# Kernel tuning notes

Measured on AMD Instinct MI355X. Metric: run time of the kernel, lower is better.

Reference implementation:

```python
import jax, jax.numpy as jnp
import numpy as np

B, T = 512, 200
N_SKILLS, M, DK, DV, H = 1000, 50, 64, 64, 128


def setup_inputs() -> dict:
    key = jax.random.key(0)
    ks = jax.random.split(key, 12)
    inp = {
        'skill_seq': jax.random.randint(ks[0], (B, T), 0, N_SKILLS, dtype=jnp.int32),
        'correct_seq': jax.random.randint(ks[1], (B, T), 0, 2, dtype=jnp.int32),
        'mask': jnp.ones((B, T), dtype=jnp.float32),
        'skill_embed': jax.random.normal(ks[2], (N_SKILLS, DK), dtype=jnp.float32),
        'key_memory': jax.random.normal(ks[3], (M, DK), dtype=jnp.float32) * 0.1,
        'value_init': jnp.zeros((M, DV), dtype=jnp.float32),
        'interaction_embed': jax.random.normal(ks[4], (2 * N_SKILLS, DV), dtype=jnp.float32),
        'erase_W': jax.random.normal(ks[5], (DV, DV), dtype=jnp.float32) * 0.05,
        'erase_b': jnp.zeros((DV,), dtype=jnp.float32),
        'add_W': jax.random.normal(ks[6], (DV, DV), dtype=jnp.float32) * 0.05,
        'add_b': jnp.zeros((DV,), dtype=jnp.float32),
        'fc1_W': jax.random.normal(ks[7], (DK + DV, H), dtype=jnp.float32) * 0.05,
        'fc1_b': jnp.zeros((H,), dtype=jnp.float32),
        'fc2_W': jax.random.normal(ks[8], (H, 1), dtype=jnp.float32) * 0.05,
        'fc2_b': jnp.zeros((1,), dtype=jnp.float32),
    }
    return inp


def reference(skill_seq, correct_seq, mask, skill_embed, key_memory, value_init,
              interaction_embed, erase_W, erase_b, add_W, add_b,
              fc1_W, fc1_b, fc2_W, fc2_b):
    n_skills = skill_embed.shape[0]
    b = skill_seq.shape[0]
    # Time-invariant-per-step quantities are precomputed vectorized over (B,T):
    q = skill_embed[skill_seq]                                   # (B,T,dk)
    w = jax.nn.softmax(jnp.einsum('btk,mk->btm', q, key_memory), axis=-1)  # (B,T,M)
    v = interaction_embed[skill_seq + correct_seq * n_skills]    # (B,T,dv)
    e = jax.nn.sigmoid(v @ erase_W + erase_b)                    # (B,T,dv)
    a = jnp.tanh(v @ add_W + add_b)                              # (B,T,dv)

    def step(mem, inputs):
        # mem: (B,M,dv); read BEFORE write, matching the torch loop
        w_t, e_t, a_t = inputs                                   # (B,M),(B,dv),(B,dv)
        read = jnp.einsum('bm,bmv->bv', w_t, mem)                # (B,dv)
        we = w_t[:, :, None]                                     # (B,M,1)
        mem = mem * (1.0 - we * e_t[:, None, :]) + we * a_t[:, None, :]
        return mem, read

    mem0 = jnp.broadcast_to(value_init, (b,) + value_init.shape)
    _, reads = jax.lax.scan(step, mem0,
                            (jnp.swapaxes(w, 0, 1), jnp.swapaxes(e, 0, 1), jnp.swapaxes(a, 0, 1)))
    reads = jnp.swapaxes(reads, 0, 1)                            # (B,T,dv)

    x = jnp.concatenate([q, reads], axis=-1)                     # (B,T,dk+dv)
    h = jax.nn.relu(x @ fc1_W + fc1_b)
    logit = (h @ fc2_W + fc2_b)[..., 0]
    p = jax.nn.sigmoid(logit)
    return p * mask, correct_seq.astype(jnp.float32) * mask
```

## Files before the change

### kernel.cpp

```cpp
#include <hip/hip_runtime.h>
#include <hip/hip_bf16.h>

#define B_  512
#define T_  200
#define NS  1000
#define M_  50
#define DK  64
#define DV  64
#define H_  128
#define NPOS (B_ * T_)

typedef __hip_bfloat16 bf16;
typedef unsigned short ushort_t;
typedef __bf16 bf16x8 __attribute__((ext_vector_type(8)));
typedef float  f32x4  __attribute__((ext_vector_type(4)));

__device__ __forceinline__ float ldf(const void* p, int i, int isbf) {
    return isbf ? __bfloat162float(((const bf16*)p)[i]) : ((const float*)p)[i];
}
__device__ __forceinline__ int sniff(const void* mask) {
    return (*(const unsigned*)mask == 0x3F800000u) ? 0 : 1;
}
__device__ __forceinline__ float rl(float x, int l) {
    return __int_as_float(__builtin_amdgcn_readlane(__float_as_int(x), l));
}
__device__ __forceinline__ ushort_t f2bf(float v) {
    bf16 h = __float2bfloat16(v);
    return *(ushort_t*)&h;
}

__global__ __launch_bounds__(256) void dk19_tabs(
    const void* __restrict__ mask,
    const void* __restrict__ skill_embed, const void* __restrict__ key_memory,
    const void* __restrict__ inter,
    const void* __restrict__ eW, const void* __restrict__ eb,
    const void* __restrict__ aW, const void* __restrict__ ab,
    const void* __restrict__ fc1W, const void* __restrict__ fc1b,
    float* __restrict__ w_tab, unsigned* __restrict__ ea_tab,
    float* __restrict__ hq_tab, ushort_t* __restrict__ W2f) {
    int isbf = sniff(mask);
    int lane = threadIdx.x & 63;
    int gwid = (blockIdx.x << 2) | (threadIdx.x >> 6);

    if (gwid < NS) {
        int s = gwid;
        float q = ldf(skill_embed, s * DK + lane, isbf);
        float acc = 0.f;
        if (lane < M_) {
            #pragma unroll 16
            for (int k = 0; k < DK; ++k)
                acc = fmaf(rl(q, k), ldf(key_memory, lane * DK + k, isbf), acc);
        }
        float val = (lane < M_) ? acc : -1e30f;
        float mx = val;
        #pragma unroll
        for (int off = 1; off < 64; off <<= 1) mx = fmaxf(mx, __shfl_xor(mx, off, 64));
        float ex = (lane < M_) ? __expf(val - mx) : 0.f;
        float sm = ex;
        #pragma unroll
        for (int off = 1; off < 64; off <<= 1) sm += __shfl_xor(sm, off, 64);
        w_tab[s * 64 + lane] = (lane < M_) ? ex / sm : 0.f;
    } else if (gwid < 3 * NS) {
        int r = gwid - NS;
        float vv = ldf(inter, r * DV + lane, isbf);
        float eacc = ldf(eb, lane, isbf);
        float aacc = ldf(ab, lane, isbf);
        #pragma unroll 16
        for (int u = 0; u < DV; ++u) {
            float vu = rl(vv, u);
            eacc = fmaf(vu, ldf(eW, u * DV + lane, isbf), eacc);
            aacc = fmaf(vu, ldf(aW, u * DV + lane, isbf), aacc);
        }
        float ev = 1.f / (1.f + __expf(-eacc));
        float av = tanhf(aacc);
        ea_tab[r * 64 + lane] = ((unsigned)f2bf(av) << 16) | (unsigned)f2bf(ev);
    } else if (gwid < 4 * NS) {
        int s = gwid - 3 * NS;
        float q = ldf(skill_embed, s * DK + lane, isbf);
        float acc0 = ldf(fc1b, lane, isbf);
        float acc1 = ldf(fc1b, 64 + lane, isbf);
        #pragma unroll 16
        for (int k = 0; k < DK; ++k) {
            float qk = rl(q, k);
            acc0 = fmaf(qk, ldf(fc1W, k * H_ + lane, isbf), acc0);
            acc1 = fmaf(qk, ldf(fc1W, k * H_ + 64 + lane, isbf), acc1);
        }
        hq_tab[s * H_ + lane]      = acc0;
        hq_tab[s * H_ + 64 + lane] = acc1;
    } else if (gwid < 4 * NS + 64) {
        int f = gwid - 4 * NS;
        int tile = f >> 3, kk = f & 7;
        int n = tile * 16 + (lane & 15);
        #pragma unroll
        for (int j = 0; j < 8; ++j) {
            int v = (kk * 32 + (lane >> 4) * 8 + j) & 63;
            W2f[(f * 64 + lane) * 8 + j] = f2bf(ldf(fc1W, (DK + v) * H_ + n, isbf));
        }
    }
}

template<int KS>
__global__ __launch_bounds__(64, 2) void dk19_scan(
    const int*  __restrict__ ss, const int* __restrict__ cs,
    const void* __restrict__ mask, const void* __restrict__ value_init,
    const float* __restrict__ w_tab, const unsigned* __restrict__ ea_tab,
    ushort_t* __restrict__ read_bf) {

    constexpr int NW = 16 / KS;
    int isbf = sniff(mask);
    int lane = threadIdx.x;
    int bk   = blockIdx.x;
    int b    = bk / KS, k = bk - b * KS;
    const int base = b * T_;
    const int row0 = (64 / KS) * k;
    const float4* w4 = (const float4*)w_tab;

    float4 mem[NW];
    #pragma unroll
    for (int i = 0; i < NW; ++i) {
        int r = row0 + 4 * i;
        mem[i].x = (r + 0 < M_) ? ldf(value_init, (r + 0) * DV + lane, isbf) : 0.f;
        mem[i].y = (r + 1 < M_) ? ldf(value_init, (r + 1) * DV + lane, isbf) : 0.f;
        mem[i].z = (r + 2 < M_) ? ldf(value_init, (r + 2) * DV + lane, isbf) : 0.f;
        mem[i].w = (r + 3 < M_) ? ldf(value_init, (r + 3) * DV + lane, isbf) : 0.f;
    }

    int s2 = ss[base + 2], c2 = cs[base + 2];
    int s3 = ss[base + 3], c3 = cs[base + 3];

    float4 wa[NW], wb[NW];
    unsigned eaA, eaB;
    {
        int sA = ss[base], cA = cs[base];
        eaA = ea_tab[(sA + cA * NS) * 64 + lane];
        #pragma unroll
        for (int i = 0; i < NW; ++i) wa[i] = w4[sA * 16 + NW * k + i];
        int sB = ss[base + 1], cB = cs[base + 1];
        eaB = ea_tab[(sB + cB * NS) * 64 + lane];
        #pragma unroll
        for (int i = 0; i < NW; ++i) wb[i] = w4[sB * 16 + NW * k + i];
    }

    for (int t = 0; t < T_; t += 2) {
        {
            float e0 = __uint_as_float(eaA << 16);
            float a0 = __uint_as_float(eaA & 0xFFFF0000u);
            float acc0 = 0.f, acc1 = 0.f, acc2 = 0.f, acc3 = 0.f;
            #pragma unroll
            for (int i = 0; i < NW; ++i) {
                float4 w = wa[i];
                acc0 = fmaf(w.x, mem[i].x, acc0);
                acc1 = fmaf(w.y, mem[i].y, acc1);
                acc2 = fmaf(w.z, mem[i].z, acc2);
                acc3 = fmaf(w.w, mem[i].w, acc3);
                mem[i].x = fmaf(-w.x, fmaf(e0, mem[i].x, -a0), mem[i].x);
                mem[i].y = fmaf(-w.y, fmaf(e0, mem[i].y, -a0), mem[i].y);
                mem[i].z = fmaf(-w.z, fmaf(e0, mem[i].z, -a0), mem[i].z);
                mem[i].w = fmaf(-w.w, fmaf(e0, mem[i].w, -a0), mem[i].w);
            }
            read_bf[((size_t)(base + t) * KS + k) * 64 + lane] =
                f2bf((acc0 + acc1) + (acc2 + acc3));
        }
        {
            eaA = ea_tab[(s2 + c2 * NS) * 64 + lane];
            #pragma unroll
            for (int i = 0; i < NW; ++i) wa[i] = w4[s2 * 16 + NW * k + i];
        }
        s2 = s3; c2 = c3;
        int tf = (t + 4 < T_) ? t + 4 : T_ - 1;
        s3 = ss[base + tf]; c3 = cs[base + tf];

        {
            float e1 = __uint_as_float(eaB << 16);
            float a1 = __uint_as_float(eaB & 0xFFFF0000u);
            float acc0 = 0.f, acc1 = 0.f, acc2 = 0.f, acc3 = 0.f;
            #pragma unroll
            for (int i = 0; i < NW; ++i) {
                float4 w = wb[i];
                acc0 = fmaf(w.x, mem[i].x, acc0);
                acc1 = fmaf(w.y, mem[i].y, acc1);
                acc2 = fmaf(w.z, mem[i].z, acc2);
                acc3 = fmaf(w.w, mem[i].w, acc3);
                mem[i].x = fmaf(-w.x, fmaf(e1, mem[i].x, -a1), mem[i].x);
                mem[i].y = fmaf(-w.y, fmaf(e1, mem[i].y, -a1), mem[i].y);
                mem[i].z = fmaf(-w.z, fmaf(e1, mem[i].z, -a1), mem[i].z);
                mem[i].w = fmaf(-w.w, fmaf(e1, mem[i].w, -a1), mem[i].w);
            }
            read_bf[((size_t)(base + t + 1) * KS + k) * 64 + lane] =
                f2bf((acc0 + acc1) + (acc2 + acc3));
        }
        {
            eaB = ea_tab[(s2 + c2 * NS) * 64 + lane];
            #pragma unroll
            for (int i = 0; i < NW; ++i) wb[i] = w4[s2 * 16 + NW * k + i];
        }
        s2 = s3; c2 = c3;
        tf = (t + 5 < T_) ? t + 5 : T_ - 1;
        s3 = ss[base + tf]; c3 = cs[base + tf];
    }
}

#define FOR8(X) X(0) X(1) X(2) X(3) X(4) X(5) X(6) X(7)
#define DECL_BT(t) bf16x8 b##t##_0, b##t##_1, b##t##_2, b##t##_3, \
                          b##t##_4, b##t##_5, b##t##_6, b##t##_7;
#define LOAD_BT(t) \
    b##t##_0 = B8[((t)*8+0)*64+lane]; b##t##_1 = B8[((t)*8+1)*64+lane]; \
    b##t##_2 = B8[((t)*8+2)*64+lane]; b##t##_3 = B8[((t)*8+3)*64+lane]; \
    b##t##_4 = B8[((t)*8+4)*64+lane]; b##t##_5 = B8[((t)*8+5)*64+lane]; \
    b##t##_6 = B8[((t)*8+6)*64+lane]; b##t##_7 = B8[((t)*8+7)*64+lane];
#define DECL_C(t)  f32x4 c##t = {0.f, 0.f, 0.f, 0.f};
#define LOAD_A(kk) bf16x8 a##kk = A8[col * 32 + (kk) * 4 + quad];
#define MFMA_KK(kk) \
    c0 = __builtin_amdgcn_mfma_f32_16x16x32_bf16(a##kk, b0_##kk, c0, 0, 0, 0); \
    c1 = __builtin_amdgcn_mfma_f32_16x16x32_bf16(a##kk, b1_##kk, c1, 0, 0, 0); \
    c2 = __builtin_amdgcn_mfma_f32_16x16x32_bf16(a##kk, b2_##kk, c2, 0, 0, 0); \
    c3 = __builtin_amdgcn_mfma_f32_16x16x32_bf16(a##kk, b3_##kk, c3, 0, 0, 0); \
    c4 = __builtin_amdgcn_mfma_f32_16x16x32_bf16(a##kk, b4_##kk, c4, 0, 0, 0); \
    c5 = __builtin_amdgcn_mfma_f32_16x16x32_bf16(a##kk, b5_##kk, c5, 0, 0, 0); \
    c6 = __builtin_amdgcn_mfma_f32_16x16x32_bf16(a##kk, b6_##kk, c6, 0, 0, 0); \
    c7 = __builtin_amdgcn_mfma_f32_16x16x32_bf16(a##kk, b7_##kk, c7, 0, 0, 0);
#define EPI(t) { \
    float h; \
    h = c##t.x + hq_tab[s0r * H_ + t * 16 + col]; x0 = fmaf(fmaxf(h, 0.f), f2w##t, x0); \
    h = c##t.y + hq_tab[s1r * H_ + t * 16 + col]; x1 = fmaf(fmaxf(h, 0.f), f2w##t, x1); \
    h = c##t.z + hq_tab[s2r * H_ + t * 16 + col]; x2 = fmaf(fmaxf(h, 0.f), f2w##t, x2); \
    h = c##t.w + hq_tab[s3r * H_ + t * 16 + col]; x3 = fmaf(fmaxf(h, 0.f), f2w##t, x3); }

__global__ __launch_bounds__(64)
__attribute__((amdgpu_waves_per_eu(1))) void dk19_fc4(
    const int*  __restrict__ skill_seq, const int* __restrict__ correct_seq,
    const void* __restrict__ mask,
    const void* __restrict__ fc2W, const void* __restrict__ fc2b,
    const float* __restrict__ hq_tab, const ushort_t* __restrict__ W2f,
    const ushort_t* __restrict__ read_bf,
    float* __restrict__ out0, float* __restrict__ out1) {

    int isbf = sniff(mask);
    int lane = threadIdx.x;
    int col  = lane & 15, quad = lane >> 4;

    const bf16x8* B8 = (const bf16x8*)W2f;
    DECL_BT(0) DECL_BT(1) DECL_BT(2) DECL_BT(3)
    DECL_BT(4) DECL_BT(5) DECL_BT(6) DECL_BT(7)
    FOR8(LOAD_BT)

    float f2w0 = ldf(fc2W,   0 + col, isbf), f2w1 = ldf(fc2W,  16 + col, isbf);
    float f2w2 = ldf(fc2W,  32 + col, isbf), f2w3 = ldf(fc2W,  48 + col, isbf);
    float f2w4 = ldf(fc2W,  64 + col, isbf), f2w5 = ldf(fc2W,  80 + col, isbf);
    float f2w6 = ldf(fc2W,  96 + col, isbf), f2w7 = ldf(fc2W, 112 + col, isbf);
    float f2b  = ldf(fc2b, 0, isbf);

    for (int pg = blockIdx.x; pg < NPOS / 16; pg += gridDim.x) {
        int p0 = pg * 16;
        const bf16x8* A8 = (const bf16x8*)(read_bf + (size_t)p0 * 256);
        LOAD_A(0) LOAD_A(1) LOAD_A(2) LOAD_A(3)
        LOAD_A(4) LOAD_A(5) LOAD_A(6) LOAD_A(7)

        int s0r = skill_seq[p0 + quad * 4 + 0];
        int s1r = skill_seq[p0 + quad * 4 + 1];
        int s2r = skill_seq[p0 + quad * 4 + 2];
        int s3r = skill_seq[p0 + quad * 4 + 3];

        FOR8(DECL_C)
        FOR8(MFMA_KK)

        float x0 = 0.f, x1 = 0.f, x2 = 0.f, x3 = 0.f;
        FOR8(EPI)

        #pragma unroll
        for (int off = 1; off < 16; off <<= 1) {
            x0 += __shfl_xor(x0, off, 64);
            x1 += __shfl_xor(x1, off, 64);
            x2 += __shfl_xor(x2, off, 64);
            x3 += __shfl_xor(x3, off, 64);
        }

        float mk0 = ldf(mask, p0 + quad * 4 + 0, isbf);
        float mk1 = ldf(mask, p0 + quad * 4 + 1, isbf);
        float mk2 = ldf(mask, p0 + quad * 4 + 2, isbf);
        float mk3 = ldf(mask, p0 + quad * 4 + 3, isbf);
        if (col == 0) {
            out0[p0 + quad * 4 + 0] = mk0 / (1.f + __expf(-(x0 + f2b)));
            out0[p0 + quad * 4 + 1] = mk1 / (1.f + __expf(-(x1 + f2b)));
            out0[p0 + quad * 4 + 2] = mk2 / (1.f + __expf(-(x2 + f2b)));
            out0[p0 + quad * 4 + 3] = mk3 / (1.f + __expf(-(x3 + f2b)));
        }
        if (col == 1) {
            out1[p0 + quad * 4 + 0] = (float)correct_seq[p0 + quad * 4 + 0] * mk0;
            out1[p0 + quad * 4 + 1] = (float)correct_seq[p0 + quad * 4 + 1] * mk1;
            out1[p0 + quad * 4 + 2] = (float)correct_seq[p0 + quad * 4 + 2] * mk2;
            out1[p0 + quad * 4 + 3] = (float)correct_seq[p0 + quad * 4 + 3] * mk3;
        }
    }
}

#define FCKK_G(kk) { \
    bf16x8 av = A8[col * (8 * KS) + (kk) * 4 + quad]; \
    c0 = __builtin_amdgcn_mfma_f32_16x16x32_bf16(av, B8[(0 * 8 + (kk)) * 64 + lane], c0, 0, 0, 0); \
    c1 = __builtin_amdgcn_mfma_f32_16x16x32_bf16(av, B8[(1 * 8 + (kk)) * 64 + lane], c1, 0, 0, 0); \
    c2 = __builtin_amdgcn_mfma_f32_16x16x32_bf16(av, B8[(2 * 8 + (kk)) * 64 + lane], c2, 0, 0, 0); \
    c3 = __builtin_amdgcn_mfma_f32_16x16x32_bf16(av, B8[(3 * 8 + (kk)) * 64 + lane], c3, 0, 0, 0); \
    c4 = __builtin_amdgcn_mfma_f32_16x16x32_bf16(av, B8[(4 * 8 + (kk)) * 64 + lane], c4, 0, 0, 0); \
    c5 = __builtin_amdgcn_mfma_f32_16x16x32_bf16(av, B8[(5 * 8 + (kk)) * 64 + lane], c5, 0, 0, 0); \
    c6 = __builtin_amdgcn_mfma_f32_16x16x32_bf16(av, B8[(6 * 8 + (kk)) * 64 + lane], c6, 0, 0, 0); \
    c7 = __builtin_amdgcn_mfma_f32_16x16x32_bf16(av, B8[(7 * 8 + (kk)) * 64 + lane], c7, 0, 0, 0); }

template<int KS>
__global__ __launch_bounds__(256) void dk19_fcgen(
    const int*  __restrict__ skill_seq, const int* __restrict__ correct_seq,
    const void* __restrict__ mask,
    const void* __restrict__ fc2W, const void* __restrict__ fc2b,
    const float* __restrict__ hq_tab, const ushort_t* __restrict__ W2f,
    const ushort_t* __restrict__ read_bf,
    float* __restrict__ out0, float* __restrict__ out1) {

    int isbf = sniff(mask);
    int lane = threadIdx.x & 63;
    int wid  = (blockIdx.x << 2) | (threadIdx.x >> 6);
    int p0   = wid * 16;
    int col  = lane & 15, quad = lane >> 4;

    const bf16x8* B8 = (const bf16x8*)W2f;
    const bf16x8* A8 = (const bf16x8*)(read_bf + (size_t)p0 * (64 * KS));

    FOR8(DECL_C)
    FCKK_G(0) FCKK_G(1) FCKK_G(2) FCKK_G(3)

    float f2w0 = ldf(fc2W,   0 + col, isbf), f2w1 = ldf(fc2W,  16 + col, isbf);
    float f2w2 = ldf(fc2W,  32 + col, isbf), f2w3 = ldf(fc2W,  48 + col, isbf);
    float f2w4 = ldf(fc2W,  64 + col, isbf), f2w5 = ldf(fc2W,  80 + col, isbf);
    float f2w6 = ldf(fc2W,  96 + col, isbf), f2w7 = ldf(fc2W, 112 + col, isbf);
    float f2b  = ldf(fc2b, 0, isbf);

    int s0r = skill_seq[p0 + quad * 4 + 0];
    int s1r = skill_seq[p0 + quad * 4 + 1];
    int s2r = skill_seq[p0 + quad * 4 + 2];
    int s3r = skill_seq[p0 + quad * 4 + 3];

    float x0 = 0.f, x1 = 0.f, x2 = 0.f, x3 = 0.f;
    FOR8(EPI)

    #pragma unroll
    for (int off = 1; off < 16; off <<= 1) {
        x0 += __shfl_xor(x0, off, 64);
        x1 += __shfl_xor(x1, off, 64);
        x2 += __shfl_xor(x2, off, 64);
        x3 += __shfl_xor(x3, off, 64);
    }

    float mk0 = ldf(mask, p0 + quad * 4 + 0, isbf);
    float mk1 = ldf(mask, p0 + quad * 4 + 1, isbf);
    float mk2 = ldf(mask, p0 + quad * 4 + 2, isbf);
    float mk3 = ldf(mask, p0 + quad * 4 + 3, isbf);
    if (col == 0) {
        out0[p0 + quad * 4 + 0] = mk0 / (1.f + __expf(-(x0 + f2b)));
        out0[p0 + quad * 4 + 1] = mk1 / (1.f + __expf(-(x1 + f2b)));
        out0[p0 + quad * 4 + 2] = mk2 / (1.f + __expf(-(x2 + f2b)));
        out0[p0 + quad * 4 + 3] = mk3 / (1.f + __expf(-(x3 + f2b)));
    }
    if (col == 1) {
        out1[p0 + quad * 4 + 0] = (float)correct_seq[p0 + quad * 4 + 0] * mk0;
        out1[p0 + quad * 4 + 1] = (float)correct_seq[p0 + quad * 4 + 1] * mk1;
        out1[p0 + quad * 4 + 2] = (float)correct_seq[p0 + quad * 4 + 2] * mk2;
        out1[p0 + quad * 4 + 3] = (float)correct_seq[p0 + quad * 4 + 3] * mk3;
    }
}

extern "C" void kernel_launch(void* const* d_in, const int* in_sizes, int n_in,
                              void* d_out, int out_size, void* d_ws, size_t ws_size,
                              hipStream_t stream) {
    const int*  skill_seq   = (const int*)d_in[0];
    const int*  correct_seq = (const int*)d_in[1];
    const void* mask        = d_in[2];
    const void* skill_embed = d_in[3];
    const void* key_memory  = d_in[4];
    const void* value_init  = d_in[5];
    const void* inter       = d_in[6];
    const void* erase_W     = d_in[7];
    const void* erase_b     = d_in[8];
    const void* add_W       = d_in[9];
    const void* add_b       = d_in[10];
    const void* fc1_W       = d_in[11];
    const void* fc1_b       = d_in[12];
    const void* fc2_W       = d_in[13];
    const void* fc2_b       = d_in[14];
    float* out = (float*)d_out;

    float*    ws      = (float*)d_ws + 16;
    float*    w_tab   = ws;
    unsigned* ea_tab  = (unsigned*)(ws + 64000);
    float*    hq_tab  = ws + 192000;
    ushort_t* W2f     = (ushort_t*)(ws + 320000);
    ushort_t* read_bf = (ushort_t*)(ws + 336400);

    dk19_tabs<<<1016, 256, 0, stream>>>(mask, skill_embed, key_memory, inter,
                                        erase_W, erase_b, add_W, add_b,
                                        fc1_W, fc1_b,
                                        w_tab, ea_tab, hq_tab, W2f);

    if (ws_size >= (size_t)54 * 1000 * 1000) {
        dk19_scan<4><<<B_ * 4, 64, 0, stream>>>(skill_seq, correct_seq, mask, value_init,
                                                w_tab, ea_tab, read_bf);
        dk19_fc4<<<1024, 64, 0, stream>>>(skill_seq, correct_seq, mask,
                                          fc2_W, fc2_b, hq_tab, W2f, read_bf,
                                          out, out + (size_t)NPOS);
    } else {
        dk19_scan<2><<<B_ * 2, 64, 0, stream>>>(skill_seq, correct_seq, mask, value_init,
                                                w_tab, ea_tab, read_bf);
        dk19_fcgen<2><<<1600, 256, 0, stream>>>(skill_seq, correct_seq, mask,
                                                fc2_W, fc2_b, hq_tab, W2f, read_bf,
                                                out, out + (size_t)NPOS);
    }
}
```

Measured before the change: 181.1 us.

## Split scan memory rows across 8 waves per batch with LDS reduction

The scan kernel now uses one 512-thread block per batch row, with 8 waves each owning 8 memory rows. Partial reads are reduced through shared memory in 8-step chunks with double buffering, so only the full fp32 read vector is written as bf16. Before, 4 separate blocks each wrote a bf16 partial that the FC kernel summed through extra K. This shrinks read_bf traffic, lets the FC kernel drop to K=64 (2 MFMAs per tile) with more waves, and removes the workspace-size fallback path. The cost is a block-wide barrier every 8 steps of a latency-bound recurrence.

```diff
diff --git a/kernel.cpp b/kernel.cpp
--- a/kernel.cpp
+++ b/kernel.cpp
@@ -29,7 +29,7 @@
     return *(ushort_t*)&h;
 }
 
-__global__ __launch_bounds__(256) void dk19_tabs(
+__global__ __launch_bounds__(256) void dk20_tabs(
     const void* __restrict__ mask,
     const void* __restrict__ skill_embed, const void* __restrict__ key_memory,
     const void* __restrict__ inter,
@@ -87,37 +87,70 @@
         }
         hq_tab[s * H_ + lane]      = acc0;
         hq_tab[s * H_ + 64 + lane] = acc1;
-    } else if (gwid < 4 * NS + 64) {
+    } else if (gwid < 4 * NS + 16) {
         int f = gwid - 4 * NS;
-        int tile = f >> 3, kk = f & 7;
+        int tile = f >> 1, kk = f & 1;
         int n = tile * 16 + (lane & 15);
         #pragma unroll
         for (int j = 0; j < 8; ++j) {
-            int v = (kk * 32 + (lane >> 4) * 8 + j) & 63;
+            int v = kk * 32 + (lane >> 4) * 8 + j;
             W2f[(f * 64 + lane) * 8 + j] = f2bf(ldf(fc1W, (DK + v) * H_ + n, isbf));
         }
     }
 }
 
-template<int KS>
-__global__ __launch_bounds__(64, 2) void dk19_scan(
+#define SCAN_STEP(EA, WARR, TP) { \
+    float e0 = __uint_as_float((EA) << 16); \
+    float a0 = __uint_as_float((EA) & 0xFFFF0000u); \
+    float acc0 = 0.f, acc1 = 0.f, acc2 = 0.f, acc3 = 0.f; \
+    _Pragma("unroll") \
+    for (int i = 0; i < 2; ++i) { \
+        float4 w = WARR[i]; \
+        acc0 = fmaf(w.x, mem[i].x, acc0); \
+        acc1 = fmaf(w.y, mem[i].y, acc1); \
+        acc2 = fmaf(w.z, mem[i].z, acc2); \
+        acc3 = fmaf(w.w, mem[i].w, acc3); \
+        mem[i].x = fmaf(-w.x, fmaf(e0, mem[i].x, -a0), mem[i].x); \
+        mem[i].y = fmaf(-w.y, fmaf(e0, mem[i].y, -a0), mem[i].y); \
+        mem[i].z = fmaf(-w.z, fmaf(e0, mem[i].z, -a0), mem[i].z); \
+        mem[i].w = fmaf(-w.w, fmaf(e0, mem[i].w, -a0), mem[i].w); \
+    } \
+    red[buf][k][TP][lane] = (acc0 + acc1) + (acc2 + acc3); }
+
+#define REFILL(EA, WARR) { \
+    EA = ea_tab[(s2 + c2 * NS) * 64 + lane]; \
+    WARR[0] = w4[s2 * 16 + 2 * k]; \
+    WARR[1] = w4[s2 * 16 + 2 * k + 1]; }
+
+#define ADV(TF) { s2 = s3; c2 = c3; int tf_ = (TF) < T_ ? (TF) : T_ - 1; \
+    s3 = ss[base + tf_]; c3 = cs[base + tf_]; }
+
+#define SUMSTORE(PB, CC) { \
+    float s_ = red[PB][0][k][lane] + red[PB][1][k][lane] \
+             + red[PB][2][k][lane] + red[PB][3][k][lane] \
+             + red[PB][4][k][lane] + red[PB][5][k][lane] \
+             + red[PB][6][k][lane] + red[PB][7][k][lane]; \
+    read_bf[(size_t)(base + (CC) * 8 + k) * 64 + lane] = f2bf(s_); }
+
+__global__ __launch_bounds__(512, 4) void dk20_scan(
     const int*  __restrict__ ss, const int* __restrict__ cs,
     const void* __restrict__ mask, const void* __restrict__ value_init,
     const float* __restrict__ w_tab, const unsigned* __restrict__ ea_tab,
     ushort_t* __restrict__ read_bf) {
 
-    constexpr int NW = 16 / KS;
+    __shared__ float red[2][8][8][64];
+
     int isbf = sniff(mask);
-    int lane = threadIdx.x;
-    int bk   = blockIdx.x;
-    int b    = bk / KS, k = bk - b * KS;
+    int lane = threadIdx.x & 63;
+    int k    = threadIdx.x >> 6;
+    int b    = blockIdx.x;
     const int base = b * T_;
-    const int row0 = (64 / KS) * k;
+    const int row0 = 8 * k;
     const float4* w4 = (const float4*)w_tab;
 
-    float4 mem[NW];
+    float4 mem[2];
     #pragma unroll
-    for (int i = 0; i < NW; ++i) {
+    for (int i = 0; i < 2; ++i) {
         int r = row0 + 4 * i;
         mem[i].x = (r + 0 < M_) ? ldf(value_init, (r + 0) * DV + lane, isbf) : 0.f;
         mem[i].y = (r + 1 < M_) ? ldf(value_init, (r + 1) * DV + lane, isbf) : 0.f;
@@ -128,97 +161,42 @@
     int s2 = ss[base + 2], c2 = cs[base + 2];
     int s3 = ss[base + 3], c3 = cs[base + 3];
 
-    float4 wa[NW], wb[NW];
+    float4 wa[2], wb[2];
     unsigned eaA, eaB;
     {
         int sA = ss[base], cA = cs[base];
         eaA = ea_tab[(sA + cA * NS) * 64 + lane];
-        #pragma unroll
-        for (int i = 0; i < NW; ++i) wa[i] = w4[sA * 16 + NW * k + i];
+        wa[0] = w4[sA * 16 + 2 * k]; wa[1] = w4[sA * 16 + 2 * k + 1];
         int sB = ss[base + 1], cB = cs[base + 1];
         eaB = ea_tab[(sB + cB * NS) * 64 + lane];
-        #pragma unroll
-        for (int i = 0; i < NW; ++i) wb[i] = w4[sB * 16 + NW * k + i];
-    }
-
-    for (int t = 0; t < T_; t += 2) {
-        {
-            float e0 = __uint_as_float(eaA << 16);
-            float a0 = __uint_as_float(eaA & 0xFFFF0000u);
-            float acc0 = 0.f, acc1 = 0.f, acc2 = 0.f, acc3 = 0.f;
-            #pragma unroll
-            for (int i = 0; i < NW; ++i) {
-                float4 w = wa[i];
-                acc0 = fmaf(w.x, mem[i].x, acc0);
-                acc1 = fmaf(w.y, mem[i].y, acc1);
-                acc2 = fmaf(w.z, mem[i].z, acc2);
-                acc3 = fmaf(w.w, mem[i].w, acc3);
-                mem[i].x = fmaf(-w.x, fmaf(e0, mem[i].x, -a0), mem[i].x);
-                mem[i].y = fmaf(-w.y, fmaf(e0, mem[i].y, -a0), mem[i].y);
-                mem[i].z = fmaf(-w.z, fmaf(e0, mem[i].z, -a0), mem[i].z);
-                mem[i].w = fmaf(-w.w, fmaf(e0, mem[i].w, -a0), mem[i].w);
-            }
-            read_bf[((size_t)(base + t) * KS + k) * 64 + lane] =
-                f2bf((acc0 + acc1) + (acc2 + acc3));
-        }
-        {
-            eaA = ea_tab[(s2 + c2 * NS) * 64 + lane];
-            #pragma unroll
-            for (int i = 0; i < NW; ++i) wa[i] = w4[s2 * 16 + NW * k + i];
-        }
-        s2 = s3; c2 = c3;
-        int tf = (t + 4 < T_) ? t + 4 : T_ - 1;
-        s3 = ss[base + tf]; c3 = cs[base + tf];
-
-        {
-            float e1 = __uint_as_float(eaB << 16);
-            float a1 = __uint_as_float(eaB & 0xFFFF0000u);
-            float acc0 = 0.f, acc1 = 0.f, acc2 = 0.f, acc3 = 0.f;
-            #pragma unroll
-            for (int i = 0; i < NW; ++i) {
-                float4 w = wb[i];
-                acc0 = fmaf(w.x, mem[i].x, acc0);
-                acc1 = fmaf(w.y, mem[i].y, acc1);
-                acc2 = fmaf(w.z, mem[i].z, acc2);
-                acc3 = fmaf(w.w, mem[i].w, acc3);
-                mem[i].x = fmaf(-w.x, fmaf(e1, mem[i].x, -a1), mem[i].x);
-                mem[i].y = fmaf(-w.y, fmaf(e1, mem[i].y, -a1), mem[i].y);
-                mem[i].z = fmaf(-w.z, fmaf(e1, mem[i].z, -a1), mem[i].z);
-                mem[i].w = fmaf(-w.w, fmaf(e1, mem[i].w, -a1), mem[i].w);
-            }
-            read_bf[((size_t)(base + t + 1) * KS + k) * 64 + lane] =
-                f2bf((acc0 + acc1) + (acc2 + acc3));
-        }
-        {
-            eaB = ea_tab[(s2 + c2 * NS) * 64 + lane];
-            #pragma unroll
-            for (int i = 0; i < NW; ++i) wb[i] = w4[s2 * 16 + NW * k + i];
-        }
-        s2 = s3; c2 = c3;
-        tf = (t + 5 < T_) ? t + 5 : T_ - 1;
-        s3 = ss[base + tf]; c3 = cs[base + tf];
-    }
+        wb[0] = w4[sB * 16 + 2 * k]; wb[1] = w4[sB * 16 + 2 * k + 1];
+    }
+
+    for (int c = 0; c < 25; ++c) {
+        int buf = c & 1;
+        #pragma unroll
+        for (int tp = 0; tp < 8; tp += 2) {
+            int t = c * 8 + tp;
+            SCAN_STEP(eaA, wa, tp)
+            REFILL(eaA, wa)
+            ADV(t + 4)
+            SCAN_STEP(eaB, wb, tp + 1)
+            REFILL(eaB, wb)
+            ADV(t + 5)
+        }
+        if (c > 0) SUMSTORE((c - 1) & 1, c - 1)
+        __syncthreads();
+    }
+    SUMSTORE(0, 24)
 }
 
 #define FOR8(X) X(0) X(1) X(2) X(3) X(4) X(5) X(6) X(7)
-#define DECL_BT(t) bf16x8 b##t##_0, b##t##_1, b##t##_2, b##t##_3, \
-                          b##t##_4, b##t##_5, b##t##_6, b##t##_7;
-#define LOAD_BT(t) \
-    b##t##_0 = B8[((t)*8+0)*64+lane]; b##t##_1 = B8[((t)*8+1)*64+lane]; \
-    b##t##_2 = B8[((t)*8+2)*64+lane]; b##t##_3 = B8[((t)*8+3)*64+lane]; \
-    b##t##_4 = B8[((t)*8+4)*64+lane]; b##t##_5 = B8[((t)*8+5)*64+lane]; \
-    b##t##_6 = B8[((t)*8+6)*64+lane]; b##t##_7 = B8[((t)*8+7)*64+lane];
 #define DECL_C(t)  f32x4 c##t = {0.f, 0.f, 0.f, 0.f};
-#define LOAD_A(kk) bf16x8 a##kk = A8[col * 32 + (kk) * 4 + quad];
-#define MFMA_KK(kk) \
-    c0 = __builtin_amdgcn_mfma_f32_16x16x32_bf16(a##kk, b0_##kk, c0, 0, 0, 0); \
-    c1 = __builtin_amdgcn_mfma_f32_16x16x32_bf16(a##kk, b1_##kk, c1, 0, 0, 0); \
-    c2 = __builtin_amdgcn_mfma_f32_16x16x32_bf16(a##kk, b2_##kk, c2, 0, 0, 0); \
-    c3 = __builtin_amdgcn_mfma_f32_16x16x32_bf16(a##kk, b3_##kk, c3, 0, 0, 0); \
-    c4 = __builtin_amdgcn_mfma_f32_16x16x32_bf16(a##kk, b4_##kk, c4, 0, 0, 0); \
-    c5 = __builtin_amdgcn_mfma_f32_16x16x32_bf16(a##kk, b5_##kk, c5, 0, 0, 0); \
-    c6 = __builtin_amdgcn_mfma_f32_16x16x32_bf16(a##kk, b6_##kk, c6, 0, 0, 0); \
-    c7 = __builtin_amdgcn_mfma_f32_16x16x32_bf16(a##kk, b7_##kk, c7, 0, 0, 0);
+#define LOADB(t) bf16x8 b##t##_0 = B8[(2 * (t)) * 64 + lane], \
+                        b##t##_1 = B8[(2 * (t) + 1) * 64 + lane];
+#define MFMA2(t) \
+    c##t = __builtin_amdgcn_mfma_f32_16x16x32_bf16(a0, b##t##_0, c##t, 0, 0, 0); \
+    c##t = __builtin_amdgcn_mfma_f32_16x16x32_bf16(a1, b##t##_1, c##t, 0, 0, 0);
 #define EPI(t) { \
     float h; \
     h = c##t.x + hq_tab[s0r * H_ + t * 16 + col]; x0 = fmaf(fmaxf(h, 0.f), f2w##t, x0); \
@@ -227,7 +205,7 @@
     h = c##t.w + hq_tab[s3r * H_ + t * 16 + col]; x3 = fmaf(fmaxf(h, 0.f), f2w##t, x3); }
 
 __global__ __launch_bounds__(64)
-__attribute__((amdgpu_waves_per_eu(1))) void dk19_fc4(
+__attribute__((amdgpu_waves_per_eu(3))) void dk20_fc(
     const int*  __restrict__ skill_seq, const int* __restrict__ correct_seq,
     const void* __restrict__ mask,
     const void* __restrict__ fc2W, const void* __restrict__ fc2b,
@@ -240,9 +218,7 @@
     int col  = lane & 15, quad = lane >> 4;
 
     const bf16x8* B8 = (const bf16x8*)W2f;
-    DECL_BT(0) DECL_BT(1) DECL_BT(2) DECL_BT(3)
-    DECL_BT(4) DECL_BT(5) DECL_BT(6) DECL_BT(7)
-    FOR8(LOAD_BT)
+    FOR8(LOADB)
 
     float f2w0 = ldf(fc2W,   0 + col, isbf), f2w1 = ldf(fc2W,  16 + col, isbf);
     float f2w2 = ldf(fc2W,  32 + col, isbf), f2w3 = ldf(fc2W,  48 + col, isbf);
@@ -252,9 +228,9 @@
 
     for (int pg = blockIdx.x; pg < NPOS / 16; pg += gridDim.x) {
         int p0 = pg * 16;
-        const bf16x8* A8 = (const bf16x8*)(read_bf + (size_t)p0 * 256);
-        LOAD_A(0) LOAD_A(1) LOAD_A(2) LOAD_A(3)
-        LOAD_A(4) LOAD_A(5) LOAD_A(6) LOAD_A(7)
+        const bf16x8* A8 = (const bf16x8*)(read_bf + (size_t)p0 * 64);
+        bf16x8 a0 = A8[col * 8 + quad];
+        bf16x8 a1 = A8[col * 8 + 4 + quad];
 
         int s0r = skill_seq[p0 + quad * 4 + 0];
         int s1r = skill_seq[p0 + quad * 4 + 1];
@@ -262,7 +238,7 @@
         int s3r = skill_seq[p0 + quad * 4 + 3];
 
         FOR8(DECL_C)
-        FOR8(MFMA_KK)
+        FOR8(MFMA2)
 
         float x0 = 0.f, x1 = 0.f, x2 = 0.f, x3 = 0.f;
         FOR8(EPI)
@@ -291,78 +267,6 @@
             out1[p0 + quad * 4 + 2] = (float)correct_seq[p0 + quad * 4 + 2] * mk2;
             out1[p0 + quad * 4 + 3] = (float)correct_seq[p0 + quad * 4 + 3] * mk3;
         }
-    }
-}
-
-#define FCKK_G(kk) { \
-    bf16x8 av = A8[col * (8 * KS) + (kk) * 4 + quad]; \
-    c0 = __builtin_amdgcn_mfma_f32_16x16x32_bf16(av, B8[(0 * 8 + (kk)) * 64 + lane], c0, 0, 0, 0); \
-    c1 = __builtin_amdgcn_mfma_f32_16x16x32_bf16(av, B8[(1 * 8 + (kk)) * 64 + lane], c1, 0, 0, 0); \
-    c2 = __builtin_amdgcn_mfma_f32_16x16x32_bf16(av, B8[(2 * 8 + (kk)) * 64 + lane], c2, 0, 0, 0); \
-    c3 = __builtin_amdgcn_mfma_f32_16x16x32_bf16(av, B8[(3 * 8 + (kk)) * 64 + lane], c3, 0, 0, 0); \
-    c4 = __builtin_amdgcn_mfma_f32_16x16x32_bf16(av, B8[(4 * 8 + (kk)) * 64 + lane], c4, 0, 0, 0); \
-    c5 = __builtin_amdgcn_mfma_f32_16x16x32_bf16(av, B8[(5 * 8 + (kk)) * 64 + lane], c5, 0, 0, 0); \
-    c6 = __builtin_amdgcn_mfma_f32_16x16x32_bf16(av, B8[(6 * 8 + (kk)) * 64 + lane], c6, 0, 0, 0); \
-    c7 = __builtin_amdgcn_mfma_f32_16x16x32_bf16(av, B8[(7 * 8 + (kk)) * 64 + lane], c7, 0, 0, 0); }
-
-template<int KS>
-__global__ __launch_bounds__(256) void dk19_fcgen(
-    const int*  __restrict__ skill_seq, const int* __restrict__ correct_seq,
-    const void* __restrict__ mask,
-    const void* __restrict__ fc2W, const void* __restrict__ fc2b,
-    const float* __restrict__ hq_tab, const ushort_t* __restrict__ W2f,
-    const ushort_t* __restrict__ read_bf,
-    float* __restrict__ out0, float* __restrict__ out1) {
-
-    int isbf = sniff(mask);
-    int lane = threadIdx.x & 63;
-    int wid  = (blockIdx.x << 2) | (threadIdx.x >> 6);
-    int p0   = wid * 16;
-    int col  = lane & 15, quad = lane >> 4;
-
-    const bf16x8* B8 = (const bf16x8*)W2f;
-    const bf16x8* A8 = (const bf16x8*)(read_bf + (size_t)p0 * (64 * KS));
-
-    FOR8(DECL_C)
-    FCKK_G(0) FCKK_G(1) FCKK_G(2) FCKK_G(3)
-
-    float f2w0 = ldf(fc2W,   0 + col, isbf), f2w1 = ldf(fc2W,  16 + col, isbf);
-    float f2w2 = ldf(fc2W,  32 + col, isbf), f2w3 = ldf(fc2W,  48 + col, isbf);
-    float f2w4 = ldf(fc2W,  64 + col, isbf), f2w5 = ldf(fc2W,  80 + col, isbf);
-    float f2w6 = ldf(fc2W,  96 + col, isbf), f2w7 = ldf(fc2W, 112 + col, isbf);
-    float f2b  = ldf(fc2b, 0, isbf);
-
-    int s0r = skill_seq[p0 + quad * 4 + 0];
-    int s1r = skill_seq[p0 + quad * 4 + 1];
-    int s2r = skill_seq[p0 + quad * 4 + 2];
-    int s3r = skill_seq[p0 + quad * 4 + 3];
-
-    float x0 = 0.f, x1 = 0.f, x2 = 0.f, x3 = 0.f;
-    FOR8(EPI)
-
-    #pragma unroll
-    for (int off = 1; off < 16; off <<= 1) {
-        x0 += __shfl_xor(x0, off, 64);
-        x1 += __shfl_xor(x1, off, 64);
-        x2 += __shfl_xor(x2, off, 64);
-        x3 += __shfl_xor(x3, off, 64);
-    }
-
-    float mk0 = ldf(mask, p0 + quad * 4 + 0, isbf);
-    float mk1 = ldf(mask, p0 + quad * 4 + 1, isbf);
-    float mk2 = ldf(mask, p0 + quad * 4 + 2, isbf);
-    float mk3 = ldf(mask, p0 + quad * 4 + 3, isbf);
-    if (col == 0) {
-        out0[p0 + quad * 4 + 0] = mk0 / (1.f + __expf(-(x0 + f2b)));
-        out0[p0 + quad * 4 + 1] = mk1 / (1.f + __expf(-(x1 + f2b)));
-        out0[p0 + quad * 4 + 2] = mk2 / (1.f + __expf(-(x2 + f2b)));
-        out0[p0 + quad * 4 + 3] = mk3 / (1.f + __expf(-(x3 + f2b)));
-    }
-    if (col == 1) {
-        out1[p0 + quad * 4 + 0] = (float)correct_seq[p0 + quad * 4 + 0] * mk0;
-        out1[p0 + quad * 4 + 1] = (float)correct_seq[p0 + quad * 4 + 1] * mk1;
-        out1[p0 + quad * 4 + 2] = (float)correct_seq[p0 + quad * 4 + 2] * mk2;
-        out1[p0 + quad * 4 + 3] = (float)correct_seq[p0 + quad * 4 + 3] * mk3;
     }
 }
 
@@ -393,22 +297,15 @@
     ushort_t* W2f     = (ushort_t*)(ws + 320000);
     ushort_t* read_bf = (ushort_t*)(ws + 336400);
 
-    dk19_tabs<<<1016, 256, 0, stream>>>(mask, skill_embed, key_memory, inter,
+    dk20_tabs<<<1004, 256, 0, stream>>>(mask, skill_embed, key_memory, inter,
                                         erase_W, erase_b, add_W, add_b,
                                         fc1_W, fc1_b,
                                         w_tab, ea_tab, hq_tab, W2f);
 
-    if (ws_size >= (size_t)54 * 1000 * 1000) {
-        dk19_scan<4><<<B_ * 4, 64, 0, stream>>>(skill_seq, correct_seq, mask, value_init,
-                                                w_tab, ea_tab, read_bf);
-        dk19_fc4<<<1024, 64, 0, stream>>>(skill_seq, correct_seq, mask,
-                                          fc2_W, fc2_b, hq_tab, W2f, read_bf,
-                                          out, out + (size_t)NPOS);
-    } else {
-        dk19_scan<2><<<B_ * 2, 64, 0, stream>>>(skill_seq, correct_seq, mask, value_init,
-                                                w_tab, ea_tab, read_bf);
-        dk19_fcgen<2><<<1600, 256, 0, stream>>>(skill_seq, correct_seq, mask,
-                                                fc2_W, fc2_b, hq_tab, W2f, read_bf,
-                                                out, out + (size_t)NPOS);
-    }
-}
+    dk20_scan<<<B_, 512, 0, stream>>>(skill_seq, correct_seq, mask, value_init,
+                                      w_tab, ea_tab, read_bf);
+
+    dk20_fc<<<3200, 64, 0, stream>>>(skill_seq, correct_seq, mask,
+                                     fc2_W, fc2_b, hq_tab, W2f, read_bf,
+                                     out, out + (size_t)NPOS);
+}
```

Measured after the change: 180.6 us. About the same (-0.3%).

## Shrink fc kernel B-register footprint, vectorize hq gathers, raise occupancy

Applied to the files above, without the earlier changes.

The fc kernel no longer holds all 64 B fragments in registers. The W2f layout now has 16 fragments, with the K offset folded via modulo in the old packing, so only 16 bf16x8 registers are kept. The hq table is stored transposed per column, so each lane fetches its 8 hq values with two float4 loads instead of 32 scalar gathers. The kernel uses waves_per_eu(3) with a 3200-block grid, and the ws_size fallback path is removed. This trades register-resident weights for higher occupancy and fewer load instructions, which risks correctness if the KS=4 read layout does not match the repacked B indexing.

```diff
diff --git a/kernel.cpp b/kernel.cpp
--- a/kernel.cpp
+++ b/kernel.cpp
@@ -29,7 +29,7 @@
     return *(ushort_t*)&h;
 }
 
-__global__ __launch_bounds__(256) void dk19_tabs(
+__global__ __launch_bounds__(256) void dk26_tabs(
     const void* __restrict__ mask,
     const void* __restrict__ skill_embed, const void* __restrict__ key_memory,
     const void* __restrict__ inter,
@@ -37,7 +37,7 @@
     const void* __restrict__ aW, const void* __restrict__ ab,
     const void* __restrict__ fc1W, const void* __restrict__ fc1b,
     float* __restrict__ w_tab, unsigned* __restrict__ ea_tab,
-    float* __restrict__ hq_tab, ushort_t* __restrict__ W2f) {
+    float* __restrict__ hq2, ushort_t* __restrict__ W2f) {
     int isbf = sniff(mask);
     int lane = threadIdx.x & 63;
     int gwid = (blockIdx.x << 2) | (threadIdx.x >> 6);
@@ -85,22 +85,22 @@
             acc0 = fmaf(qk, ldf(fc1W, k * H_ + lane, isbf), acc0);
             acc1 = fmaf(qk, ldf(fc1W, k * H_ + 64 + lane, isbf), acc1);
         }
-        hq_tab[s * H_ + lane]      = acc0;
-        hq_tab[s * H_ + 64 + lane] = acc1;
-    } else if (gwid < 4 * NS + 64) {
+        hq2[s * H_ + (lane & 15) * 8 +     (lane >> 4)] = acc0;
+        hq2[s * H_ + (lane & 15) * 8 + 4 + (lane >> 4)] = acc1;
+    } else if (gwid < 4 * NS + 16) {
         int f = gwid - 4 * NS;
-        int tile = f >> 3, kk = f & 7;
+        int tile = f >> 1, kk = f & 1;
         int n = tile * 16 + (lane & 15);
         #pragma unroll
         for (int j = 0; j < 8; ++j) {
-            int v = (kk * 32 + (lane >> 4) * 8 + j) & 63;
+            int v = kk * 32 + (lane >> 4) * 8 + j;
             W2f[(f * 64 + lane) * 8 + j] = f2bf(ldf(fc1W, (DK + v) * H_ + n, isbf));
         }
     }
 }
 
 template<int KS>
-__global__ __launch_bounds__(64, 2) void dk19_scan(
+__global__ __launch_bounds__(64, 2) void dk26_scan(
     const int*  __restrict__ ss, const int* __restrict__ cs,
     const void* __restrict__ mask, const void* __restrict__ value_init,
     const float* __restrict__ w_tab, const unsigned* __restrict__ ea_tab,
@@ -201,37 +201,33 @@
 }
 
 #define FOR8(X) X(0) X(1) X(2) X(3) X(4) X(5) X(6) X(7)
-#define DECL_BT(t) bf16x8 b##t##_0, b##t##_1, b##t##_2, b##t##_3, \
-                          b##t##_4, b##t##_5, b##t##_6, b##t##_7;
-#define LOAD_BT(t) \
-    b##t##_0 = B8[((t)*8+0)*64+lane]; b##t##_1 = B8[((t)*8+1)*64+lane]; \
-    b##t##_2 = B8[((t)*8+2)*64+lane]; b##t##_3 = B8[((t)*8+3)*64+lane]; \
-    b##t##_4 = B8[((t)*8+4)*64+lane]; b##t##_5 = B8[((t)*8+5)*64+lane]; \
-    b##t##_6 = B8[((t)*8+6)*64+lane]; b##t##_7 = B8[((t)*8+7)*64+lane];
 #define DECL_C(t)  f32x4 c##t = {0.f, 0.f, 0.f, 0.f};
-#define LOAD_A(kk) bf16x8 a##kk = A8[col * 32 + (kk) * 4 + quad];
-#define MFMA_KK(kk) \
-    c0 = __builtin_amdgcn_mfma_f32_16x16x32_bf16(a##kk, b0_##kk, c0, 0, 0, 0); \
-    c1 = __builtin_amdgcn_mfma_f32_16x16x32_bf16(a##kk, b1_##kk, c1, 0, 0, 0); \
-    c2 = __builtin_amdgcn_mfma_f32_16x16x32_bf16(a##kk, b2_##kk, c2, 0, 0, 0); \
-    c3 = __builtin_amdgcn_mfma_f32_16x16x32_bf16(a##kk, b3_##kk, c3, 0, 0, 0); \
-    c4 = __builtin_amdgcn_mfma_f32_16x16x32_bf16(a##kk, b4_##kk, c4, 0, 0, 0); \
-    c5 = __builtin_amdgcn_mfma_f32_16x16x32_bf16(a##kk, b5_##kk, c5, 0, 0, 0); \
-    c6 = __builtin_amdgcn_mfma_f32_16x16x32_bf16(a##kk, b6_##kk, c6, 0, 0, 0); \
-    c7 = __builtin_amdgcn_mfma_f32_16x16x32_bf16(a##kk, b7_##kk, c7, 0, 0, 0);
+#define LOADB(t) bf16x8 b##t##_0 = B8[(2 * (t)) * 64 + lane], \
+                        b##t##_1 = B8[(2 * (t) + 1) * 64 + lane];
+#define FCKK(kk, p) { \
+    bf16x8 av = A8[col * 32 + (kk) * 4 + quad]; \
+    c0 = __builtin_amdgcn_mfma_f32_16x16x32_bf16(av, b0_##p, c0, 0, 0, 0); \
+    c1 = __builtin_amdgcn_mfma_f32_16x16x32_bf16(av, b1_##p, c1, 0, 0, 0); \
+    c2 = __builtin_amdgcn_mfma_f32_16x16x32_bf16(av, b2_##p, c2, 0, 0, 0); \
+    c3 = __builtin_amdgcn_mfma_f32_16x16x32_bf16(av, b3_##p, c3, 0, 0, 0); \
+    c4 = __builtin_amdgcn_mfma_f32_16x16x32_bf16(av, b4_##p, c4, 0, 0, 0); \
+    c5 = __builtin_amdgcn_mfma_f32_16x16x32_bf16(av, b5_##p, c5, 0, 0, 0); \
+    c6 = __builtin_amdgcn_mfma_f32_16x16x32_bf16(av, b6_##p, c6, 0, 0, 0); \
+    c7 = __builtin_amdgcn_mfma_f32_16x16x32_bf16(av, b7_##p, c7, 0, 0, 0); }
+#define HQ(r, t) (((t) < 4) ? qa##r[(t) & 3] : qb##r[(t) & 3])
 #define EPI(t) { \
     float h; \
-    h = c##t.x + hq_tab[s0r * H_ + t * 16 + col]; x0 = fmaf(fmaxf(h, 0.f), f2w##t, x0); \
-    h = c##t.y + hq_tab[s1r * H_ + t * 16 + col]; x1 = fmaf(fmaxf(h, 0.f), f2w##t, x1); \
-    h = c##t.z + hq_tab[s2r * H_ + t * 16 + col]; x2 = fmaf(fmaxf(h, 0.f), f2w##t, x2); \
-    h = c##t.w + hq_tab[s3r * H_ + t * 16 + col]; x3 = fmaf(fmaxf(h, 0.f), f2w##t, x3); }
+    h = c##t.x + HQ(0, t); x0 = fmaf(fmaxf(h, 0.f), f2w##t, x0); \
+    h = c##t.y + HQ(1, t); x1 = fmaf(fmaxf(h, 0.f), f2w##t, x1); \
+    h = c##t.z + HQ(2, t); x2 = fmaf(fmaxf(h, 0.f), f2w##t, x2); \
+    h = c##t.w + HQ(3, t); x3 = fmaf(fmaxf(h, 0.f), f2w##t, x3); }
 
 __global__ __launch_bounds__(64)
-__attribute__((amdgpu_waves_per_eu(1))) void dk19_fc4(
+__attribute__((amdgpu_waves_per_eu(3))) void dk26_fc(
     const int*  __restrict__ skill_seq, const int* __restrict__ correct_seq,
     const void* __restrict__ mask,
     const void* __restrict__ fc2W, const void* __restrict__ fc2b,
-    const float* __restrict__ hq_tab, const ushort_t* __restrict__ W2f,
+    const float* __restrict__ hq2, const ushort_t* __restrict__ W2f,
     const ushort_t* __restrict__ read_bf,
     float* __restrict__ out0, float* __restrict__ out1) {
 
@@ -240,9 +236,7 @@
     int col  = lane & 15, quad = lane >> 4;
 
     const bf16x8* B8 = (const bf16x8*)W2f;
-    DECL_BT(0) DECL_BT(1) DECL_BT(2) DECL_BT(3)
-    DECL_BT(4) DECL_BT(5) DECL_BT(6) DECL_BT(7)
-    FOR8(LOAD_BT)
+    FOR8(LOADB)
 
     float f2w0 = ldf(fc2W,   0 + col, isbf), f2w1 = ldf(fc2W,  16 + col, isbf);
     float f2w2 = ldf(fc2W,  32 + col, isbf), f2w3 = ldf(fc2W,  48 + col, isbf);
@@ -253,16 +247,24 @@
     for (int pg = blockIdx.x; pg < NPOS / 16; pg += gridDim.x) {
         int p0 = pg * 16;
         const bf16x8* A8 = (const bf16x8*)(read_bf + (size_t)p0 * 256);
-        LOAD_A(0) LOAD_A(1) LOAD_A(2) LOAD_A(3)
-        LOAD_A(4) LOAD_A(5) LOAD_A(6) LOAD_A(7)
 
         int s0r = skill_seq[p0 + quad * 4 + 0];
         int s1r = skill_seq[p0 + quad * 4 + 1];
         int s2r = skill_seq[p0 + quad * 4 + 2];
         int s3r = skill_seq[p0 + quad * 4 + 3];
 
+        f32x4 qa0 = *(const f32x4*)(hq2 + s0r * H_ + col * 8);
+        f32x4 qb0 = *(const f32x4*)(hq2 + s0r * H_ + col * 8 + 4);
+        f32x4 qa1 = *(const f32x4*)(hq2 + s1r * H_ + col * 8);
+        f32x4 qb1 = *(const f32x4*)(hq2 + s1r * H_ + col * 8 + 4);
+        f32x4 qa2 = *(const f32x4*)(hq2 + s2r * H_ + col * 8);
+        f32x4 qb2 = *(const f32x4*)(hq2 + s2r * H_ + col * 8 + 4);
+        f32x4 qa3 = *(const f32x4*)(hq2 + s3r * H_ + col * 8);
+        f32x4 qb3 = *(const f32x4*)(hq2 + s3r * H_ + col * 8 + 4);
+
         FOR8(DECL_C)
-        FOR8(MFMA_KK)
+        FCKK(0, 0) FCKK(1, 1) FCKK(2, 0) FCKK(3, 1)
+        FCKK(4, 0) FCKK(5, 1) FCKK(6, 0) FCKK(7, 1)
 
         float x0 = 0.f, x1 = 0.f, x2 = 0.f, x3 = 0.f;
         FOR8(EPI)
@@ -291,78 +293,6 @@
             out1[p0 + quad * 4 + 2] = (float)correct_seq[p0 + quad * 4 + 2] * mk2;
             out1[p0 + quad * 4 + 3] = (float)correct_seq[p0 + quad * 4 + 3] * mk3;
         }
-    }
-}
-
-#define FCKK_G(kk) { \
-    bf16x8 av = A8[col * (8 * KS) + (kk) * 4 + quad]; \
-    c0 = __builtin_amdgcn_mfma_f32_16x16x32_bf16(av, B8[(0 * 8 + (kk)) * 64 + lane], c0, 0, 0, 0); \
-    c1 = __builtin_amdgcn_mfma_f32_16x16x32_bf16(av, B8[(1 * 8 + (kk)) * 64 + lane], c1, 0, 0, 0); \
-    c2 = __builtin_amdgcn_mfma_f32_16x16x32_bf16(av, B8[(2 * 8 + (kk)) * 64 + lane], c2, 0, 0, 0); \
-    c3 = __builtin_amdgcn_mfma_f32_16x16x32_bf16(av, B8[(3 * 8 + (kk)) * 64 + lane], c3, 0, 0, 0); \
-    c4 = __builtin_amdgcn_mfma_f32_16x16x32_bf16(av, B8[(4 * 8 + (kk)) * 64 + lane], c4, 0, 0, 0); \
-    c5 = __builtin_amdgcn_mfma_f32_16x16x32_bf16(av, B8[(5 * 8 + (kk)) * 64 + lane], c5, 0, 0, 0); \
-    c6 = __builtin_amdgcn_mfma_f32_16x16x32_bf16(av, B8[(6 * 8 + (kk)) * 64 + lane], c6, 0, 0, 0); \
-    c7 = __builtin_amdgcn_mfma_f32_16x16x32_bf16(av, B8[(7 * 8 + (kk)) * 64 + lane], c7, 0, 0, 0); }
-
-template<int KS>
-__global__ __launch_bounds__(256) void dk19_fcgen(
-    const int*  __restrict__ skill_seq, const int* __restrict__ correct_seq,
-    const void* __restrict__ mask,
-    const void* __restrict__ fc2W, const void* __restrict__ fc2b,
-    const float* __restrict__ hq_tab, const ushort_t* __restrict__ W2f,
-    const ushort_t* __restrict__ read_bf,
-    float* __restrict__ out0, float* __restrict__ out1) {
-
-    int isbf = sniff(mask);
-    int lane = threadIdx.x & 63;
-    int wid  = (blockIdx.x << 2) | (threadIdx.x >> 6);
-    int p0   = wid * 16;
-    int col  = lane & 15, quad = lane >> 4;
-
-    const bf16x8* B8 = (const bf16x8*)W2f;
-    const bf16x8* A8 = (const bf16x8*)(read_bf + (size_t)p0 * (64 * KS));
-
-    FOR8(DECL_C)
-    FCKK_G(0) FCKK_G(1) FCKK_G(2) FCKK_G(3)
-
-    float f2w0 = ldf(fc2W,   0 + col, isbf), f2w1 = ldf(fc2W,  16 + col, isbf);
-    float f2w2 = ldf(fc2W,  32 + col, isbf), f2w3 = ldf(fc2W,  48 + col, isbf);
-    float f2w4 = ldf(fc2W,  64 + col, isbf), f2w5 = ldf(fc2W,  80 + col, isbf);
-    float f2w6 = ldf(fc2W,  96 + col, isbf), f2w7 = ldf(fc2W, 112 + col, isbf);
-    float f2b  = ldf(fc2b, 0, isbf);
-
-    int s0r = skill_seq[p0 + quad * 4 + 0];
-    int s1r = skill_seq[p0 + quad * 4 + 1];
-    int s2r = skill_seq[p0 + quad * 4 + 2];
-    int s3r = skill_seq[p0 + quad * 4 + 3];
-
-    float x0 = 0.f, x1 = 0.f, x2 = 0.f, x3 = 0.f;
-    FOR8(EPI)
-
-    #pragma unroll
-    for (int off = 1; off < 16; off <<= 1) {
-        x0 += __shfl_xor(x0, off, 64);
-        x1 += __shfl_xor(x1, off, 64);
-        x2 += __shfl_xor(x2, off, 64);
-        x3 += __shfl_xor(x3, off, 64);
-    }
-
-    float mk0 = ldf(mask, p0 + quad * 4 + 0, isbf);
-    float mk1 = ldf(mask, p0 + quad * 4 + 1, isbf);
-    float mk2 = ldf(mask, p0 + quad * 4 + 2, isbf);
-    float mk3 = ldf(mask, p0 + quad * 4 + 3, isbf);
-    if (col == 0) {
-        out0[p0 + quad * 4 + 0] = mk0 / (1.f + __expf(-(x0 + f2b)));
-        out0[p0 + quad * 4 + 1] = mk1 / (1.f + __expf(-(x1 + f2b)));
-        out0[p0 + quad * 4 + 2] = mk2 / (1.f + __expf(-(x2 + f2b)));
-        out0[p0 + quad * 4 + 3] = mk3 / (1.f + __expf(-(x3 + f2b)));
-    }
-    if (col == 1) {
-        out1[p0 + quad * 4 + 0] = (float)correct_seq[p0 + quad * 4 + 0] * mk0;
-        out1[p0 + quad * 4 + 1] = (float)correct_seq[p0 + quad * 4 + 1] * mk1;
-        out1[p0 + quad * 4 + 2] = (float)correct_seq[p0 + quad * 4 + 2] * mk2;
-        out1[p0 + quad * 4 + 3] = (float)correct_seq[p0 + quad * 4 + 3] * mk3;
     }
 }
 
@@ -389,26 +319,19 @@
     float*    ws      = (float*)d_ws + 16;
     float*    w_tab   = ws;
     unsigned* ea_tab  = (unsigned*)(ws + 64000);
-    float*    hq_tab  = ws + 192000;
+    float*    hq2     = ws + 192000;
     ushort_t* W2f     = (ushort_t*)(ws + 320000);
     ushort_t* read_bf = (ushort_t*)(ws + 336400);
 
-    dk19_tabs<<<1016, 256, 0, stream>>>(mask, skill_embed, key_memory, inter,
+    dk26_tabs<<<1004, 256, 0, stream>>>(mask, skill_embed, key_memory, inter,
                                         erase_W, erase_b, add_W, add_b,
                                         fc1_W, fc1_b,
-                                        w_tab, ea_tab, hq_tab, W2f);
-
-    if (ws_size >= (size_t)54 * 1000 * 1000) {
-        dk19_scan<4><<<B_ * 4, 64, 0, stream>>>(skill_seq, correct_seq, mask, value_init,
-                                                w_tab, ea_tab, read_bf);
-        dk19_fc4<<<1024, 64, 0, stream>>>(skill_seq, correct_seq, mask,
-                                          fc2_W, fc2_b, hq_tab, W2f, read_bf,
-                                          out, out + (size_t)NPOS);
-    } else {
-        dk19_scan<2><<<B_ * 2, 64, 0, stream>>>(skill_seq, correct_seq, mask, value_init,
-                                                w_tab, ea_tab, read_bf);
-        dk19_fcgen<2><<<1600, 256, 0, stream>>>(skill_seq, correct_seq, mask,
-                                                fc2_W, fc2_b, hq_tab, W2f, read_bf,
-                                                out, out + (size_t)NPOS);
-    }
-}
+                                        w_tab, ea_tab, hq2, W2f);
+
+    dk26_scan<4><<<B_ * 4, 64, 0, stream>>>(skill_seq, correct_seq, mask, value_init,
+                                            w_tab, ea_tab, read_bf);
+
+    dk26_fc<<<3200, 64, 0, stream>>>(skill_seq, correct_seq, mask,
+                                     fc2_W, fc2_b, hq2, W2f, read_bf,
+                                     out, out + (size_t)NPOS);
+}
```

Result: no change. 180.2 us (-0.5%).
